# Kernel tuning notes

Hardware: AMD Instinct MI355X
Metric: run time of the kernel (lower is better)

The kernel has to match this reference:

```python
import jax, jax.numpy as jnp
import numpy as np
from jax import lax

BETA = 5.0
THRESHOLD = 20.0

def softplus5(x):
    # torch nn.Softplus(beta=5, threshold=20)
    return jnp.where(BETA * x > THRESHOLD, x, jax.nn.softplus(BETA * x) / BETA)

def setup_inputs() -> dict:
    key = jax.random.key(0)
    k1, k2, k3, k4, k5 = jax.random.split(key, 5)
    B, T, I, H = 128, 256, 1024, 1024
    stdv = 1.0 / np.sqrt(H)
    x = jax.random.normal(k1, (B, T, I), dtype=jnp.float32)
    hidden = jnp.zeros((2, B, H), dtype=jnp.float32)
    Wi = jax.random.uniform(k2, (H, I), dtype=jnp.float32, minval=-stdv, maxval=stdv)
    bi = jax.random.uniform(k3, (H,), dtype=jnp.float32, minval=-stdv, maxval=stdv)
    Wh = jax.random.uniform(k4, (H, H), dtype=jnp.float32, minval=-stdv, maxval=stdv)
    bh = jax.random.uniform(k5, (H,), dtype=jnp.float32, minval=-stdv, maxval=stdv)
    return {"x": x, "hidden": hidden, "Wi": Wi, "bi": bi, "Wh": Wh, "bh": bh}

def reference(x, hidden, Wi, bi, Wh, bh):
    # x: [B, T, I] (batch_first) -> time-major [T, B, I]
    xt = jnp.swapaxes(x, 0, 1)
    T = xt.shape[0]
    # precompute i2h for all steps (one big GEMM)
    pre = jnp.einsum('tbi,hi->tbh', xt, Wi) + bi  # [T, B, H]

    def step(h, p):
        h_next = softplus5(p + h @ Wh.T + bh)
        return h_next, h_next

    _, fwd = lax.scan(step, hidden[0], pre)          # fwd[t]: hidden after step t
    _, bwd = lax.scan(step, hidden[1], pre[::-1])    # bwd[j]: backward hidden at time i = T-1-j
    # bi_outputs appended for i = T-1 ... 0: position t holds cat(outputs[(T-1-t)-16], bwd[t])
    idx = (jnp.arange(T)[::-1] - 16) % T  # Python negative-index wrap of outputs[i-16]
    out = jnp.concatenate([fwd[idx], bwd], axis=-1)  # [T, B, 2H]
    return jnp.swapaxes(out, 0, 1)                   # [B, T, 2H]
```

## Files before the change

### kernel.cpp

```cpp
#include <hip/hip_runtime.h>
#include <stddef.h>

using short8 = __attribute__((ext_vector_type(8))) short;
using f32x4  = __attribute__((ext_vector_type(4))) float;
using f32x16 = __attribute__((ext_vector_type(16))) float;
using u16x4  = __attribute__((ext_vector_type(4))) unsigned short;

__device__ __forceinline__ unsigned short cvt_bf16(float f) {
    unsigned u = __builtin_bit_cast(unsigned, f);
    u += 0x7fffu + ((u >> 16) & 1u);
    return (unsigned short)(u >> 16);
}

__device__ __forceinline__ void gload_lds16(const void* g, void* l) {
    __builtin_amdgcn_global_load_lds(
        (const __attribute__((address_space(1))) unsigned*)g,
        (__attribute__((address_space(3))) unsigned*)l, 16, 0, 0);
}

#define MFMA16(a, b, c) __builtin_amdgcn_mfma_f32_16x16x32_bf16((a), (b), (c), 0, 0, 0)
#define MFMA32(a, b, c) __builtin_amdgcn_mfma_f32_32x32x16_bf16((a), (b), (c), 0, 0, 0)

__global__ __launch_bounds__(256) void convert_w(const float* __restrict__ Wi,
                                                 const float* __restrict__ Wh,
                                                 unsigned short* __restrict__ Wib,
                                                 unsigned short* __restrict__ Whb) {
    const float* src = blockIdx.y ? Wh : Wi;
    unsigned short* dst = blockIdx.y ? Whb : Wib;
    int base = blockIdx.x * 2048 + threadIdx.x * 8;
#pragma unroll
    for (int c = 0; c < 2; ++c) {
        float4 v = *(const float4*)(src + base + c * 4);
        u16x4 o;
        o.x = cvt_bf16(v.x); o.y = cvt_bf16(v.y); o.z = cvt_bf16(v.z); o.w = cvt_bf16(v.w);
        *(u16x4*)(dst + base + c * 4) = o;
    }
}

__global__ __launch_bounds__(256) void init_h(const float* __restrict__ hidden,
                                              unsigned short* __restrict__ h0,
                                              unsigned* __restrict__ flags) {
    int row = blockIdx.x;
    int tid = threadIdx.x;
    float4 v = *(const float4*)(hidden + (size_t)row * 1024 + tid * 4);
    u16x4 o;
    o.x = cvt_bf16(v.x); o.y = cvt_bf16(v.y); o.z = cvt_bf16(v.z); o.w = cvt_bf16(v.w);
    *(u16x4*)(h0 + (size_t)row * 1024 + tid * 4) = o;
    if (blockIdx.x == 0 && tid < 256) flags[tid] = 0;
}

__global__ __launch_bounds__(256) void pre_gemm(const float* __restrict__ x,
                                                const unsigned short* __restrict__ Wib,
                                                const float* __restrict__ bi,
                                                float* __restrict__ pre) {
    __shared__ unsigned short Alds[128 * 64];
    __shared__ unsigned short Blds[128 * 64];
    const int tid  = threadIdx.x;
    const int lane = tid & 63, wid = tid >> 6;
    const int wr = wid >> 1, wc = wid & 1;
    const int t  = blockIdx.y;
    const int n0 = blockIdx.x * 128;

    f32x4 acc[4][4] = {};

    for (int kt = 0; kt < 16; ++kt) {
        const int k0 = kt * 64;
        __syncthreads();
#pragma unroll
        for (int c = 0; c < 8; ++c) {
            int flat = c * 256 + tid;
            int row = flat >> 4;
            int seg = flat & 15;
            float4 v = *(const float4*)(x + (size_t)row * 262144 + (size_t)t * 1024 + k0 + seg * 4);
            u16x4 h;
            h.x = cvt_bf16(v.x); h.y = cvt_bf16(v.y); h.z = cvt_bf16(v.z); h.w = cvt_bf16(v.w);
            *(u16x4*)&Alds[row * 64 + seg * 4] = h;
        }
#pragma unroll
        for (int c = 0; c < 4; ++c) {
            int flat = c * 256 + tid;
            int row = flat >> 3;
            int seg = flat & 7;
            gload_lds16(Wib + (size_t)(n0 + row) * 1024 + k0 + seg * 8, &Blds[flat * 8]);
        }
        __syncthreads();
#pragma unroll
        for (int ks = 0; ks < 2; ++ks) {
            short8 a[4], b[4];
#pragma unroll
            for (int i = 0; i < 4; ++i)
                a[i] = *(const short8*)&Alds[(wr * 64 + i * 16 + (lane & 15)) * 64 + ks * 32 + (lane >> 4) * 8];
#pragma unroll
            for (int j = 0; j < 4; ++j)
                b[j] = *(const short8*)&Blds[(wc * 64 + j * 16 + (lane & 15)) * 64 + ks * 32 + (lane >> 4) * 8];
#pragma unroll
            for (int i = 0; i < 4; ++i)
#pragma unroll
                for (int j = 0; j < 4; ++j)
                    acc[i][j] = MFMA16(a[i], b[j], acc[i][j]);
        }
    }
    const int rbase = wr * 64 + (lane >> 4) * 4;
    const int cbase = n0 + wc * 64 + (lane & 15);
#pragma unroll
    for (int i = 0; i < 4; ++i) {
#pragma unroll
        for (int j = 0; j < 4; ++j) {
            int n = cbase + j * 16;
            float bv = bi[n];
#pragma unroll
            for (int r = 0; r < 4; ++r) {
                int m = rbase + i * 16 + r;
                pre[((size_t)t * 128 + m) * 1024 + n] = acc[i][j][r] + bv;
            }
        }
    }
}

__global__ __launch_bounds__(256, 1) void rnn_scan(const unsigned short* __restrict__ Whb,
                                                   const float* __restrict__ pre,
                                                   const float* __restrict__ bh,
                                                   unsigned short* __restrict__ ha,
                                                   unsigned short* __restrict__ hb,
                                                   float* __restrict__ out,
                                                   unsigned* __restrict__ flags) {
    __shared__ unsigned short Alds[32 * 1024];
    __shared__ float Red[4][1024];

    const int tid  = threadIdx.x;
    const int lane = tid & 63, wid = tid >> 6;
    const int bid  = blockIdx.x;
    const int g    = bid & 7, ni = bid >> 3;
    const int m0   = g * 32, n0 = ni * 32;
    const bool fwd = (g < 4);
    unsigned* gflags = flags + g * 32;

    short8 bfrag[16];
    {
        const unsigned short* bp = Whb + (size_t)(n0 + (lane & 31)) * 1024
                                 + wid * 256 + (lane >> 5) * 8;
#pragma unroll
        for (int ks = 0; ks < 16; ++ks)
            bfrag[ks] = *(const short8*)(bp + ks * 16);
    }

    const int mloc = tid >> 3;
    const int nloc = (tid & 7) * 4;
    const int m    = m0 + mloc;
    const int b    = m & 127;
    const int n    = n0 + nloc;
    const float4 bh4 = *(const float4*)(bh + n);
    float* outp      = out + (size_t)b * 524288 + (fwd ? 0 : 1024) + n;
    const float* prebase = pre + (size_t)b * 1024 + n;

    const char* aswz_base = (const char*)Alds + (lane & 31) * 2048;
    const int   aswz      = (lane & 7) << 4;
    const int   kb0       = wid * 512 + (lane >> 5) * 16;

    for (int s = 0; s < 256; ++s) {
        const unsigned short* hin = (s & 1) ? hb : ha;
        unsigned short* hout      = (s & 1) ? ha : hb;
        const int prow = fwd ? s : 255 - s;
        float4 pv = *(const float4*)(prebase + (size_t)prow * 131072);

        if (s > 0) {
            if (tid < 64) {
                int fuel = 1 << 20;
                unsigned v;
                do {
                    v = __hip_atomic_load(&gflags[lane & 31], __ATOMIC_RELAXED,
                                          __HIP_MEMORY_SCOPE_AGENT);
                } while (!__all((int)(v >= (unsigned)s)) && --fuel);
            }
            __syncthreads();
        }

        {
            const unsigned long long* hsrc =
                (const unsigned long long*)(hin + (size_t)m0 * 1024);
            const int colswz = tid * 8;
            unsigned long long tmp[32];
#pragma unroll
            for (int i = 0; i < 32; ++i)
                tmp[i] = __hip_atomic_load(&hsrc[(size_t)i * 256 + tid],
                                           __ATOMIC_RELAXED, __HIP_MEMORY_SCOPE_AGENT);
#pragma unroll
            for (int i = 0; i < 32; ++i)
                *(unsigned long long*)((char*)Alds + i * 2048
                                       + (colswz ^ ((i & 7) << 4))) = tmp[i];
        }
        __syncthreads();

        f32x16 acc0 = {}, acc1 = {};
#pragma unroll
        for (int ks = 0; ks < 16; ++ks) {
            short8 a = *(const short8*)(aswz_base + ((kb0 + ks * 32) ^ aswz));
            if (ks & 1) acc1 = MFMA32(a, bfrag[ks], acc1);
            else        acc0 = MFMA32(a, bfrag[ks], acc0);
        }
        f32x16 acc = acc0 + acc1;
#pragma unroll
        for (int r = 0; r < 16; ++r) {
            int row = (r & 3) + 8 * (r >> 2) + 4 * (lane >> 5);
            Red[wid][row * 32 + (lane & 31)] = acc[r];
        }
        __syncthreads();

        f32x4 ov;
        {
            const int o = tid * 4;
            float4 q0 = *(const float4*)&Red[0][o];
            float4 q1 = *(const float4*)&Red[1][o];
            float4 q2 = *(const float4*)&Red[2][o];
            float4 q3 = *(const float4*)&Red[3][o];
            float vv[4] = { q0.x + q1.x + q2.x + q3.x + pv.x + bh4.x,
                            q0.y + q1.y + q2.y + q3.y + pv.y + bh4.y,
                            q0.z + q1.z + q2.z + q3.z + pv.z + bh4.z,
                            q0.w + q1.w + q2.w + q3.w + pv.w + bh4.w };
            u16x4 hh;
#pragma unroll
            for (int j = 0; j < 4; ++j) {
                float xv = vv[j];
                float hv = (5.0f * xv > 20.0f) ? xv : 0.2f * log1pf(__expf(5.0f * xv));
                ov[j] = hv;
                hh[j] = cvt_bf16(hv);
            }
            __hip_atomic_store((unsigned long long*)(hout + (size_t)m * 1024 + n),
                               __builtin_bit_cast(unsigned long long, hh),
                               __ATOMIC_RELAXED, __HIP_MEMORY_SCOPE_AGENT);
        }
        asm volatile("s_waitcnt vmcnt(0)" ::: "memory");
        __syncthreads();

        if (s < 255 && tid == 0)
            __hip_atomic_store(&gflags[ni], (unsigned)(s + 1),
                               __ATOMIC_RELAXED, __HIP_MEMORY_SCOPE_AGENT);

        int tout = fwd ? ((239 - s) & 255) : s;
        __builtin_nontemporal_store(ov, (f32x4*)(outp + (size_t)tout * 2048));
    }
}

extern "C" void kernel_launch(void* const* d_in, const int* in_sizes, int n_in,
                              void* d_out, int out_size, void* d_ws, size_t ws_size,
                              hipStream_t stream) {
    const float* x      = (const float*)d_in[0];
    const float* hidden = (const float*)d_in[1];
    const float* Wi     = (const float*)d_in[2];
    const float* bi     = (const float*)d_in[3];
    const float* Wh     = (const float*)d_in[4];
    const float* bh     = (const float*)d_in[5];
    float* out = (float*)d_out;

    char* ws = (char*)d_ws;
    float*          pre = (float*)ws;
    unsigned short* Wib = (unsigned short*)(ws + 134217728);
    unsigned short* Whb = (unsigned short*)(ws + 136314880);
    unsigned short* ha  = (unsigned short*)(ws + 138412032);
    unsigned short* hb  = (unsigned short*)(ws + 138936320);
    unsigned*     flags = (unsigned*)(ws + 139460608);

    convert_w<<<dim3(512, 2), 256, 0, stream>>>(Wi, Wh, Wib, Whb);
    init_h<<<256, 256, 0, stream>>>(hidden, ha, flags);
    pre_gemm<<<dim3(8, 256), 256, 0, stream>>>(x, Wib, bi, pre);
    rnn_scan<<<256, 256, 0, stream>>>(Whb, pre, bh, ha, hb, out, flags);
}
```

Before: 1.214 ms.

## Fuse forward and backward scans into one block per batch group

The recurrent scan moves from 256 blocks, each handling one direction, to 128 blocks that each run both the forward and the backward recurrence for the same batch rows and output columns. Each block reuses its register-resident Wh fragments for both directions and loads both hidden-state tiles up front, so the backward loads overlap the forward compute. The flag array doubles so one 64-lane poll covers both directions' producers. In exchange, each block now runs two MFMA/reduce/activation phases back to back per timestep, which lengthens the per-step critical path and leaves half the CUs idle.

```diff
diff --git a/kernel.cpp b/kernel.cpp
--- a/kernel.cpp
+++ b/kernel.cpp
@@ -5,6 +5,7 @@
 using f32x4  = __attribute__((ext_vector_type(4))) float;
 using f32x16 = __attribute__((ext_vector_type(16))) float;
 using u16x4  = __attribute__((ext_vector_type(4))) unsigned short;
+using u64    = unsigned long long;
 
 __device__ __forceinline__ unsigned short cvt_bf16(float f) {
     unsigned u = __builtin_bit_cast(unsigned, f);
@@ -46,7 +47,9 @@
     u16x4 o;
     o.x = cvt_bf16(v.x); o.y = cvt_bf16(v.y); o.z = cvt_bf16(v.z); o.w = cvt_bf16(v.w);
     *(u16x4*)(h0 + (size_t)row * 1024 + tid * 4) = o;
-    if (blockIdx.x == 0 && tid < 256) flags[tid] = 0;
+    if (blockIdx.x == 0) {
+        for (int i = tid; i < 512; i += 256) flags[i] = 0;
+    }
 }
 
 __global__ __launch_bounds__(256) void pre_gemm(const float* __restrict__ x,
@@ -124,16 +127,18 @@
                                                    unsigned short* __restrict__ hb,
                                                    float* __restrict__ out,
                                                    unsigned* __restrict__ flags) {
-    __shared__ unsigned short Alds[32 * 1024];
+    __shared__ unsigned short AldsF[32 * 1024];
+    __shared__ unsigned short AldsB[32 * 1024];
     __shared__ float Red[4][1024];
 
     const int tid  = threadIdx.x;
     const int lane = tid & 63, wid = tid >> 6;
     const int bid  = blockIdx.x;
-    const int g    = bid & 7, ni = bid >> 3;
-    const int m0   = g * 32, n0 = ni * 32;
-    const bool fwd = (g < 4);
-    unsigned* gflags = flags + g * 32;
+    const int g    = bid & 3, ni = bid >> 2;
+    const int m0f  = g * 32;
+    const int m0b  = 128 + g * 32;
+    const int n0   = ni * 32;
+    unsigned* gflags = flags + g * 64;
 
     short8 bfrag[16];
     {
@@ -146,98 +151,150 @@
 
     const int mloc = tid >> 3;
     const int nloc = (tid & 7) * 4;
-    const int m    = m0 + mloc;
-    const int b    = m & 127;
+    const int bb   = m0f + mloc;
     const int n    = n0 + nloc;
     const float4 bh4 = *(const float4*)(bh + n);
-    float* outp      = out + (size_t)b * 524288 + (fwd ? 0 : 1024) + n;
-    const float* prebase = pre + (size_t)b * 1024 + n;
-
-    const char* aswz_base = (const char*)Alds + (lane & 31) * 2048;
-    const int   aswz      = (lane & 7) << 4;
-    const int   kb0       = wid * 512 + (lane >> 5) * 16;
+    const float* prebase = pre + (size_t)bb * 1024 + n;
+    float* outF = out + (size_t)bb * 524288 + n;
+    float* outB = out + (size_t)bb * 524288 + 1024 + n;
+
+    const int   kb0   = wid * 512 + (lane >> 5) * 16;
+    const int   aswz  = (lane & 7) << 4;
+    const char* arowF = (const char*)AldsF + (lane & 31) * 2048;
+    const char* arowB = (const char*)AldsB + (lane & 31) * 2048;
+    const int   colswz = tid * 8;
 
     for (int s = 0; s < 256; ++s) {
         const unsigned short* hin = (s & 1) ? hb : ha;
         unsigned short* hout      = (s & 1) ? ha : hb;
-        const int prow = fwd ? s : 255 - s;
-        float4 pv = *(const float4*)(prebase + (size_t)prow * 131072);
+
+        float4 pvF = *(const float4*)(prebase + (size_t)s * 131072);
+        float4 pvB = *(const float4*)(prebase + (size_t)(255 - s) * 131072);
 
         if (s > 0) {
-            if (tid < 64) {
-                int fuel = 1 << 20;
-                unsigned v;
-                do {
-                    v = __hip_atomic_load(&gflags[lane & 31], __ATOMIC_RELAXED,
-                                          __HIP_MEMORY_SCOPE_AGENT);
-                } while (!__all((int)(v >= (unsigned)s)) && --fuel);
-            }
-            __syncthreads();
-        }
-
-        {
-            const unsigned long long* hsrc =
-                (const unsigned long long*)(hin + (size_t)m0 * 1024);
-            const int colswz = tid * 8;
-            unsigned long long tmp[32];
-#pragma unroll
-            for (int i = 0; i < 32; ++i)
-                tmp[i] = __hip_atomic_load(&hsrc[(size_t)i * 256 + tid],
-                                           __ATOMIC_RELAXED, __HIP_MEMORY_SCOPE_AGENT);
-#pragma unroll
-            for (int i = 0; i < 32; ++i)
-                *(unsigned long long*)((char*)Alds + i * 2048
-                                       + (colswz ^ ((i & 7) << 4))) = tmp[i];
-        }
-        __syncthreads();
-
-        f32x16 acc0 = {}, acc1 = {};
-#pragma unroll
-        for (int ks = 0; ks < 16; ++ks) {
-            short8 a = *(const short8*)(aswz_base + ((kb0 + ks * 32) ^ aswz));
-            if (ks & 1) acc1 = MFMA32(a, bfrag[ks], acc1);
-            else        acc0 = MFMA32(a, bfrag[ks], acc0);
-        }
-        f32x16 acc = acc0 + acc1;
-#pragma unroll
-        for (int r = 0; r < 16; ++r) {
-            int row = (r & 3) + 8 * (r >> 2) + 4 * (lane >> 5);
-            Red[wid][row * 32 + (lane & 31)] = acc[r];
-        }
-        __syncthreads();
-
-        f32x4 ov;
+            int fuel = 1 << 22;
+            unsigned v;
+            do {
+                v = __hip_atomic_load(&gflags[lane], __ATOMIC_RELAXED,
+                                      __HIP_MEMORY_SCOPE_AGENT);
+            } while (!__all((int)(v >= (unsigned)s)) && --fuel);
+        }
+
+        const u64* hsF = (const u64*)(hin + (size_t)m0f * 1024);
+        const u64* hsB = (const u64*)(hin + (size_t)m0b * 1024);
+        u64 tF[32], tB[32];
+#pragma unroll
+        for (int i = 0; i < 32; ++i)
+            tF[i] = __hip_atomic_load(&hsF[(size_t)i * 256 + tid],
+                                      __ATOMIC_RELAXED, __HIP_MEMORY_SCOPE_AGENT);
+#pragma unroll
+        for (int i = 0; i < 32; ++i)
+            tB[i] = __hip_atomic_load(&hsB[(size_t)i * 256 + tid],
+                                      __ATOMIC_RELAXED, __HIP_MEMORY_SCOPE_AGENT);
+
+#pragma unroll
+        for (int i = 0; i < 32; ++i)
+            *(u64*)((char*)AldsF + i * 2048 + (colswz ^ ((i & 7) << 4))) = tF[i];
+        __syncthreads();
+
+        {
+            f32x16 acc0 = {}, acc1 = {};
+#pragma unroll
+            for (int ks = 0; ks < 16; ++ks) {
+                short8 a = *(const short8*)(arowF + ((kb0 + ks * 32) ^ aswz));
+                if (ks & 1) acc1 = MFMA32(a, bfrag[ks], acc1);
+                else        acc0 = MFMA32(a, bfrag[ks], acc0);
+            }
+            f32x16 acc = acc0 + acc1;
+#pragma unroll
+            for (int r = 0; r < 16; ++r) {
+                int row = (r & 3) + 8 * (r >> 2) + 4 * (lane >> 5);
+                Red[wid][row * 32 + (lane & 31)] = acc[r];
+            }
+        }
+        __syncthreads();
+
+        f32x4 ovF;
         {
             const int o = tid * 4;
-            float4 q0 = *(const float4*)&Red[0][o];
-            float4 q1 = *(const float4*)&Red[1][o];
-            float4 q2 = *(const float4*)&Red[2][o];
-            float4 q3 = *(const float4*)&Red[3][o];
-            float vv[4] = { q0.x + q1.x + q2.x + q3.x + pv.x + bh4.x,
-                            q0.y + q1.y + q2.y + q3.y + pv.y + bh4.y,
-                            q0.z + q1.z + q2.z + q3.z + pv.z + bh4.z,
-                            q0.w + q1.w + q2.w + q3.w + pv.w + bh4.w };
+            f32x4 q0 = *(const f32x4*)&Red[0][o];
+            f32x4 q1 = *(const f32x4*)&Red[1][o];
+            f32x4 q2 = *(const f32x4*)&Red[2][o];
+            f32x4 q3 = *(const f32x4*)&Red[3][o];
+            f32x4 vv = q0 + q1 + q2 + q3;
             u16x4 hh;
 #pragma unroll
             for (int j = 0; j < 4; ++j) {
-                float xv = vv[j];
+                float xv = vv[j] + ((const float*)&pvF)[j] + ((const float*)&bh4)[j];
                 float hv = (5.0f * xv > 20.0f) ? xv : 0.2f * log1pf(__expf(5.0f * xv));
-                ov[j] = hv;
+                ovF[j] = hv;
                 hh[j] = cvt_bf16(hv);
             }
-            __hip_atomic_store((unsigned long long*)(hout + (size_t)m * 1024 + n),
-                               __builtin_bit_cast(unsigned long long, hh),
+            __hip_atomic_store((u64*)(hout + (size_t)(m0f + mloc) * 1024 + n),
+                               __builtin_bit_cast(u64, hh),
                                __ATOMIC_RELAXED, __HIP_MEMORY_SCOPE_AGENT);
         }
         asm volatile("s_waitcnt vmcnt(0)" ::: "memory");
         __syncthreads();
-
-        if (s < 255 && tid == 0)
+        if (tid == 0 && s < 255)
             __hip_atomic_store(&gflags[ni], (unsigned)(s + 1),
                                __ATOMIC_RELAXED, __HIP_MEMORY_SCOPE_AGENT);
-
-        int tout = fwd ? ((239 - s) & 255) : s;
-        __builtin_nontemporal_store(ov, (f32x4*)(outp + (size_t)tout * 2048));
+        {
+            const int toutF = (239 - s) & 255;
+            __builtin_nontemporal_store(ovF, (f32x4*)(outF + (size_t)toutF * 2048));
+        }
+
+#pragma unroll
+        for (int i = 0; i < 32; ++i)
+            *(u64*)((char*)AldsB + i * 2048 + (colswz ^ ((i & 7) << 4))) = tB[i];
+        __syncthreads();
+
+        {
+            f32x16 acc0 = {}, acc1 = {};
+#pragma unroll
+            for (int ks = 0; ks < 16; ++ks) {
+                short8 a = *(const short8*)(arowB + ((kb0 + ks * 32) ^ aswz));
+                if (ks & 1) acc1 = MFMA32(a, bfrag[ks], acc1);
+                else        acc0 = MFMA32(a, bfrag[ks], acc0);
+            }
+            f32x16 acc = acc0 + acc1;
+#pragma unroll
+            for (int r = 0; r < 16; ++r) {
+                int row = (r & 3) + 8 * (r >> 2) + 4 * (lane >> 5);
+                Red[wid][row * 32 + (lane & 31)] = acc[r];
+            }
+        }
+        __syncthreads();
+
+        f32x4 ovB;
+        {
+            const int o = tid * 4;
+            f32x4 q0 = *(const f32x4*)&Red[0][o];
+            f32x4 q1 = *(const f32x4*)&Red[1][o];
+            f32x4 q2 = *(const f32x4*)&Red[2][o];
+            f32x4 q3 = *(const f32x4*)&Red[3][o];
+            f32x4 vv = q0 + q1 + q2 + q3;
+            u16x4 hh;
+#pragma unroll
+            for (int j = 0; j < 4; ++j) {
+                float xv = vv[j] + ((const float*)&pvB)[j] + ((const float*)&bh4)[j];
+                float hv = (5.0f * xv > 20.0f) ? xv : 0.2f * log1pf(__expf(5.0f * xv));
+                ovB[j] = hv;
+                hh[j] = cvt_bf16(hv);
+            }
+            __hip_atomic_store((u64*)(hout + (size_t)(m0b + mloc) * 1024 + n),
+                               __builtin_bit_cast(u64, hh),
+                               __ATOMIC_RELAXED, __HIP_MEMORY_SCOPE_AGENT);
+        }
+        asm volatile("s_waitcnt vmcnt(0)" ::: "memory");
+        __syncthreads();
+        if (tid == 0 && s < 255)
+            __hip_atomic_store(&gflags[32 + ni], (unsigned)(s + 1),
+                               __ATOMIC_RELAXED, __HIP_MEMORY_SCOPE_AGENT);
+        {
+            const int toutB = s;
+            __builtin_nontemporal_store(ovB, (f32x4*)(outB + (size_t)toutB * 2048));
+        }
     }
 }
 
@@ -263,5 +320,5 @@
     convert_w<<<dim3(512, 2), 256, 0, stream>>>(Wi, Wh, Wib, Whb);
     init_h<<<256, 256, 0, stream>>>(hidden, ha, flags);
     pre_gemm<<<dim3(8, 256), 256, 0, stream>>>(x, Wib, bi, pre);
-    rnn_scan<<<256, 256, 0, stream>>>(Whb, pre, bh, ha, hb, out, flags);
-}
+    rnn_scan<<<128, 256, 0, stream>>>(Whb, pre, bh, ha, hb, out, flags);
+}
```

New measurement: 2.029 ms. 67.1% more time.
